# Performance work log

Measured on AMD Instinct MI355X. Metric: run time of the kernel, lower is better.

Reference implementation:

```python
import jax, jax.numpy as jnp
import numpy as np

N_NODES = 100000
N_EDGES = 250000
IN_CH = 256
OUT_CH = 256
REL_DIM = 1536
N_REL = 64
HIDDEN = IN_CH * 2  # 512
EPS = 1e-5


def setup_inputs() -> dict:
    key = jax.random.key(0)
    ks = jax.random.split(key, 12)
    s = 0.02
    return {
        "x": jax.random.normal(ks[0], (N_NODES, IN_CH), jnp.float32),
        "edge_index": jax.random.randint(ks[1], (2, N_EDGES), 0, N_NODES, jnp.int64),
        "edge_type": jax.random.randint(ks[2], (N_EDGES,), 0, N_REL, jnp.int64),
        "relation_embs": jax.random.normal(ks[3], (N_REL, REL_DIM), jnp.float32),
        "W1": jax.random.normal(ks[4], (IN_CH + REL_DIM, HIDDEN), jnp.float32) * s,
        "b1": jnp.zeros((HIDDEN,), jnp.float32),
        "W2": jax.random.normal(ks[5], (HIDDEN, OUT_CH), jnp.float32) * s,
        "b2": jnp.zeros((OUT_CH,), jnp.float32),
        "Ws": jax.random.normal(ks[6], (IN_CH, OUT_CH), jnp.float32) * s,
        "bs": jnp.zeros((OUT_CH,), jnp.float32),
        "gamma": jnp.ones((OUT_CH,), jnp.float32),
        "beta": jnp.zeros((OUT_CH,), jnp.float32),
    }


def reference(x, edge_index, edge_type, relation_embs, W1, b1, W2, b2, Ws, bs, gamma, beta):
    src, dst = edge_index[0], edge_index[1]
    # gather: per-edge inputs [E, in+rel]
    msg_in = jnp.concatenate([x[src], relation_embs[edge_type]], axis=-1)
    # message MLP: Linear -> ReLU -> Linear
    h = jax.nn.relu(msg_in @ W1 + b1)
    messages = h @ W2 + b2  # [E, out]
    # scatter_add into destination nodes
    agg = jax.ops.segment_sum(messages, dst, num_segments=x.shape[0])
    out = x @ Ws + bs + agg
    # LayerNorm (eps=1e-5) then ReLU
    mu = jnp.mean(out, axis=-1, keepdims=True)
    var = jnp.mean(jnp.square(out - mu), axis=-1, keepdims=True)
    out = (out - mu) * jax.lax.rsqrt(var + EPS) * gamma + beta
    return jax.nn.relu(out)
```

## Files before the change

### kernel.cpp

```cpp
#include <hip/hip_runtime.h>
#include <hip/hip_bf16.h>

#define IN_CHN 256
#define OUT_CHN 256
#define REL_DIM 1536
#define HIDN 512

using short8 = __attribute__((ext_vector_type(8))) short;
using f32x4  = __attribute__((ext_vector_type(4))) float;

__device__ __forceinline__ float bf2f(short s) {
    union { unsigned u; float f; } v;
    v.u = ((unsigned)(unsigned short)s) << 16;
    return v.f;
}
__device__ __forceinline__ unsigned cvt_pk_bf16(float a, float b) {
    unsigned r;
    asm("v_cvt_pk_bf16_f32 %0, %1, %2" : "=v"(r) : "v"(a), "v"(b));
    return r;
}
__device__ __forceinline__ unsigned short f2bf_s(float f) {
    union { float f; unsigned u; } v; v.f = f;
    unsigned u = v.u + 0x7FFFu + ((v.u >> 16) & 1u);
    return (unsigned short)(u >> 16);
}

__global__ void k_prep_w(const float* __restrict__ W1, const float* __restrict__ Ws,
                         const float* __restrict__ W2,
                         unsigned short* __restrict__ Bt, unsigned short* __restrict__ W2t,
                         unsigned short* __restrict__ Wst)
{
    int idx = blockIdx.x * 256 + threadIdx.x;
    const int n1 = HIDN * IN_CHN;
    const int n2 = OUT_CHN * HIDN;
    const int n3 = OUT_CHN * IN_CHN;
    if (idx < n1) {
        int j = idx >> 8, k = idx & 255;
        Bt[idx] = f2bf_s(W1[(size_t)k * HIDN + j]);
    } else if (idx < n1 + n2) {
        int t = idx - n1;
        int j = t >> 9, k = t & 511;
        W2t[t] = f2bf_s(W2[(size_t)k * OUT_CHN + j]);
    } else if (idx < n1 + n2 + n3) {
        int t = idx - n1 - n2;
        int j = t >> 8, k = t & 255;
        Wst[t] = f2bf_s(Ws[(size_t)k * OUT_CHN + j]);
    }
}

__global__ __launch_bounds__(512) void k_rel(const float* __restrict__ rel,
                                             const float* __restrict__ W1,
                                             const float* __restrict__ b1,
                                             unsigned short* __restrict__ Rb)
{
    __shared__ float s[REL_DIM];
    const int r = blockIdx.x;
    for (int i = threadIdx.x; i < REL_DIM; i += 512)
        s[i] = rel[(size_t)r * REL_DIM + i];
    __syncthreads();
    const int j = threadIdx.x;
    float acc = b1[j];
    const float* wp = W1 + (size_t)IN_CHN * HIDN + j;
#pragma unroll 8
    for (int k = 0; k < REL_DIM; ++k)
        acc = fmaf(s[k], wp[(size_t)k * HIDN], acc);
    Rb[r * HIDN + j] = f2bf_s(acc);
}

__global__ __launch_bounds__(256) void k_node(const float* __restrict__ x,
                                              const unsigned short* __restrict__ Bt,
                                              unsigned short* __restrict__ X1, int N)
{
    __shared__ unsigned short Alds[64][72];
    const int row0 = blockIdx.x * 64;
    const int colb = blockIdx.y * 256;
    const int tid = threadIdx.x;
    const int w = tid >> 6, l = tid & 63;
    const int l15 = l & 15, lg = l >> 4;
    const int colw = colb + w * 64;

    const int srow = tid >> 2;
    int srowg = row0 + srow; if (srowg >= N) srowg = N - 1;
    const int sc = (tid & 3) * 16;
    const float* xsrc = x + (size_t)srowg * IN_CHN + sc;
    unsigned short* sdst0 = &Alds[srow][sc];
    unsigned short* sdst1 = &Alds[srow][sc + 8];

    const unsigned short* bp[4];
#pragma unroll
    for (int cf = 0; cf < 4; ++cf)
        bp[cf] = Bt + (size_t)(colw + 16 * cf + l15) * IN_CHN + 8 * lg;
    const unsigned short* ard[4];
#pragma unroll
    for (int rf = 0; rf < 4; ++rf)
        ard[rf] = &Alds[16 * rf + l15][lg * 8];

    f32x4 acc[4][4] = {};

    {
        float4 f0 = *(const float4*)(xsrc + 0);
        float4 f1 = *(const float4*)(xsrc + 4);
        float4 f2 = *(const float4*)(xsrc + 8);
        float4 f3 = *(const float4*)(xsrc + 12);
        union { short8 s; unsigned u[4]; } p0, p1;
        p0.u[0] = cvt_pk_bf16(f0.x, f0.y); p0.u[1] = cvt_pk_bf16(f0.z, f0.w);
        p0.u[2] = cvt_pk_bf16(f1.x, f1.y); p0.u[3] = cvt_pk_bf16(f1.z, f1.w);
        p1.u[0] = cvt_pk_bf16(f2.x, f2.y); p1.u[1] = cvt_pk_bf16(f2.z, f2.w);
        p1.u[2] = cvt_pk_bf16(f3.x, f3.y); p1.u[3] = cvt_pk_bf16(f3.z, f3.w);
        *(short8*)sdst0 = p0.s;
        *(short8*)sdst1 = p1.s;
    }
    __syncthreads();
    for (int t = 0; t < 4; ++t) {
        float4 f0, f1, f2, f3;
        if (t + 1 < 4) {
            f0 = *(const float4*)(xsrc + (t + 1) * 64);
            f1 = *(const float4*)(xsrc + (t + 1) * 64 + 4);
            f2 = *(const float4*)(xsrc + (t + 1) * 64 + 8);
            f3 = *(const float4*)(xsrc + (t + 1) * 64 + 12);
        }
#pragma unroll
        for (int kk = 0; kk < 2; ++kk) {
            short8 a[4], b[4];
#pragma unroll
            for (int rf = 0; rf < 4; ++rf)
                a[rf] = *(const short8*)(ard[rf] + kk * 32);
#pragma unroll
            for (int cf = 0; cf < 4; ++cf)
                b[cf] = *(const short8*)(bp[cf] + t * 64 + kk * 32);
#pragma unroll
            for (int rf = 0; rf < 4; ++rf)
#pragma unroll
                for (int cf = 0; cf < 4; ++cf)
                    acc[rf][cf] = __builtin_amdgcn_mfma_f32_16x16x32_bf16(a[rf], b[cf], acc[rf][cf], 0, 0, 0);
        }
        __syncthreads();
        if (t + 1 < 4) {
            union { short8 s; unsigned u[4]; } p0, p1;
            p0.u[0] = cvt_pk_bf16(f0.x, f0.y); p0.u[1] = cvt_pk_bf16(f0.z, f0.w);
            p0.u[2] = cvt_pk_bf16(f1.x, f1.y); p0.u[3] = cvt_pk_bf16(f1.z, f1.w);
            p1.u[0] = cvt_pk_bf16(f2.x, f2.y); p1.u[1] = cvt_pk_bf16(f2.z, f2.w);
            p1.u[2] = cvt_pk_bf16(f3.x, f3.y); p1.u[3] = cvt_pk_bf16(f3.z, f3.w);
            *(short8*)sdst0 = p0.s;
            *(short8*)sdst1 = p1.s;
            __syncthreads();
        }
    }

#pragma unroll
    for (int rf = 0; rf < 4; ++rf) {
#pragma unroll
        for (int cf = 0; cf < 4; ++cf) {
            int col = colw + 16 * cf + l15;
#pragma unroll
            for (int r = 0; r < 4; ++r) {
                int row = row0 + 16 * rf + 4 * lg + r;
                if (row >= N) continue;
                X1[(size_t)row * HIDN + col] = f2bf_s(acc[rf][cf][r]);
            }
        }
    }
}

__global__ void k_hist(const int* __restrict__ ei, int* __restrict__ cnt, int E)
{
    int e = blockIdx.x * 256 + threadIdx.x;
    if (e < E) atomicAdd(&cnt[ei[E + e]], 1);
}

__global__ __launch_bounds__(512) void k_scan1(const int* __restrict__ cnt, int* __restrict__ offs,
                                               int* __restrict__ bsum, int N)
{
    __shared__ int s[512];
    int t = threadIdx.x;
    int i = blockIdx.x * 512 + t;
    int v = (i < N) ? cnt[i] : 0;
    s[t] = v;
    __syncthreads();
    for (int d = 1; d < 512; d <<= 1) {
        int a = (t >= d) ? s[t - d] : 0;
        __syncthreads();
        s[t] += a;
        __syncthreads();
    }
    if (i < N) offs[i] = s[t] - v;
    if (t == 511) bsum[blockIdx.x] = s[511];
}

__global__ __launch_bounds__(512) void k_scan2(int* __restrict__ bsum, int NB)
{
    __shared__ int s[512];
    int t = threadIdx.x;
    if (t < NB) s[t] = bsum[t];
    __syncthreads();
    if (t == 0) {
        int run = 0;
        for (int j = 0; j < NB; ++j) { int v = s[j]; s[j] = run; run += v; }
    }
    __syncthreads();
    if (t < NB) bsum[t] = s[t];
}

__global__ void k_scan3(int* __restrict__ offs, const int* __restrict__ bsum,
                        int* __restrict__ cursor, int N, int E)
{
    int i = blockIdx.x * 256 + threadIdx.x;
    if (i < N) {
        int v = offs[i] + bsum[i >> 9];
        offs[i] = v;
        cursor[i] = v;
    }
    if (i == 0) offs[N] = E;
}

__global__ void k_scatter(const int* __restrict__ ei, const int* __restrict__ et,
                          int* __restrict__ cursor, int* __restrict__ eperm, int E)
{
    int e = blockIdx.x * 256 + threadIdx.x;
    if (e < E) {
        int d = ei[E + e];
        int pos = atomicAdd(&cursor[d], 1);
        eperm[pos] = ei[e] | (et[e] << 20);
    }
}

__global__ __launch_bounds__(256, 6) void k_gather(const int* __restrict__ offs,
                                                   const int* __restrict__ eperm,
                                                   const unsigned short* __restrict__ X1,
                                                   const unsigned short* __restrict__ Rb,
                                                   unsigned short* __restrict__ Hagg, int N)
{
    const int g = (blockIdx.x * 256 + threadIdx.x) >> 6;
    const int l = threadIdx.x & 63;
    if (g >= N) return;
    const int o0 = offs[g], o1 = offs[g + 1];
    const int deg = o1 - o0;
    float a8[8] = {};
    for (int base = 0; base < deg; base += 64) {
        const int nk = min(64, deg - base);
        int pv = eperm[o0 + base + (l < nk ? l : nk - 1)];
        for (int e = 0; e < nk; e += 4) {
            int pvk[4];
#pragma unroll
            for (int k2 = 0; k2 < 4; ++k2)
                pvk[k2] = __shfl(pv, e + k2);
            short8 xa[4], ra[4];
#pragma unroll
            for (int k2 = 0; k2 < 4; ++k2) {
                if (e + k2 < nk) {
                    xa[k2] = *(const short8*)(X1 + (size_t)(pvk[k2] & 0xFFFFF) * HIDN + l * 8);
                    ra[k2] = *(const short8*)(Rb + (pvk[k2] >> 20) * HIDN + l * 8);
                }
            }
#pragma unroll
            for (int k2 = 0; k2 < 4; ++k2) {
                if (e + k2 < nk) {
#pragma unroll
                    for (int j = 0; j < 8; ++j)
                        a8[j] += fmaxf(bf2f(xa[k2][j]) + bf2f(ra[k2][j]), 0.f);
                }
            }
        }
    }
    union { short8 s; unsigned u[4]; } pk;
    pk.u[0] = cvt_pk_bf16(a8[0], a8[1]);
    pk.u[1] = cvt_pk_bf16(a8[2], a8[3]);
    pk.u[2] = cvt_pk_bf16(a8[4], a8[5]);
    pk.u[3] = cvt_pk_bf16(a8[6], a8[7]);
    *(short8*)(Hagg + (size_t)g * HIDN + l * 8) = pk.s;
}

__global__ __launch_bounds__(256) void k_out(const unsigned short* __restrict__ Hagg,
                                             const unsigned short* __restrict__ W2t,
                                             const unsigned short* __restrict__ Wst,
                                             const float* __restrict__ x,
                                             const int* __restrict__ offs,
                                             const float* __restrict__ b2,
                                             const float* __restrict__ bs,
                                             const float* __restrict__ gamma,
                                             const float* __restrict__ beta,
                                             float* __restrict__ out, int N)
{
    __shared__ unsigned short Alds[64][72];
    __shared__ float sdeg[64];
    __shared__ float sred[4][64], sqred[4][64];
    const int row0 = blockIdx.x * 64;
    const int tid = threadIdx.x;
    const int w = tid >> 6, l = tid & 63;
    const int l15 = l & 15, lg = l >> 4;
    const int colw = w * 64;

    if (tid < 64) {
        int g = row0 + tid;
        if (g >= N) g = N - 1;
        sdeg[tid] = (float)(offs[g + 1] - offs[g]);
    }

    const int srow = tid >> 2;
    int srowg = row0 + srow; if (srowg >= N) srowg = N - 1;
    const int sc = (tid & 3) * 16;
    const unsigned short* hsrc = Hagg + (size_t)srowg * HIDN + sc;
    const float* xsrc = x + (size_t)srowg * IN_CHN + sc;
    unsigned short* sdst0 = &Alds[srow][sc];
    unsigned short* sdst1 = &Alds[srow][sc + 8];

    const unsigned short* bp[4];
    const unsigned short* sp[4];
#pragma unroll
    for (int cf = 0; cf < 4; ++cf) {
        bp[cf] = W2t + (size_t)(colw + 16 * cf + l15) * HIDN + 8 * lg;
        sp[cf] = Wst + (size_t)(colw + 16 * cf + l15) * IN_CHN + 8 * lg;
    }
    const unsigned short* ard[4];
#pragma unroll
    for (int rf = 0; rf < 4; ++rf)
        ard[rf] = &Alds[16 * rf + l15][lg * 8];

    f32x4 acc[4][4] = {};
    short8 st0, st1;

    st0 = *(const short8*)(hsrc + 0);
    st1 = *(const short8*)(hsrc + 8);
    *(short8*)sdst0 = st0;
    *(short8*)sdst1 = st1;
    __syncthreads();
    for (int t = 0; t < 8; ++t) {
        if (t + 1 < 8) {
            st0 = *(const short8*)(hsrc + (t + 1) * 64);
            st1 = *(const short8*)(hsrc + (t + 1) * 64 + 8);
        }
#pragma unroll
        for (int kk = 0; kk < 2; ++kk) {
            short8 a[4], b[4];
#pragma unroll
            for (int rf = 0; rf < 4; ++rf)
                a[rf] = *(const short8*)(ard[rf] + kk * 32);
#pragma unroll
            for (int cf = 0; cf < 4; ++cf)
                b[cf] = *(const short8*)(bp[cf] + t * 64 + kk * 32);
#pragma unroll
            for (int rf = 0; rf < 4; ++rf)
#pragma unroll
                for (int cf = 0; cf < 4; ++cf)
                    acc[rf][cf] = __builtin_amdgcn_mfma_f32_16x16x32_bf16(a[rf], b[cf], acc[rf][cf], 0, 0, 0);
        }
        __syncthreads();
        if (t + 1 < 8) {
            *(short8*)sdst0 = st0;
            *(short8*)sdst1 = st1;
            __syncthreads();
        }
    }

    {
        float4 f0 = *(const float4*)(xsrc + 0);
        float4 f1 = *(const float4*)(xsrc + 4);
        float4 f2 = *(const float4*)(xsrc + 8);
        float4 f3 = *(const float4*)(xsrc + 12);
        union { short8 s; unsigned u[4]; } p0, p1;
        p0.u[0] = cvt_pk_bf16(f0.x, f0.y); p0.u[1] = cvt_pk_bf16(f0.z, f0.w);
        p0.u[2] = cvt_pk_bf16(f1.x, f1.y); p0.u[3] = cvt_pk_bf16(f1.z, f1.w);
        p1.u[0] = cvt_pk_bf16(f2.x, f2.y); p1.u[1] = cvt_pk_bf16(f2.z, f2.w);
        p1.u[2] = cvt_pk_bf16(f3.x, f3.y); p1.u[3] = cvt_pk_bf16(f3.z, f3.w);
        *(short8*)sdst0 = p0.s;
        *(short8*)sdst1 = p1.s;
    }
    __syncthreads();
    for (int t = 0; t < 4; ++t) {
        float4 f0, f1, f2, f3;
        if (t + 1 < 4) {
            f0 = *(const float4*)(xsrc + (t + 1) * 64);
            f1 = *(const float4*)(xsrc + (t + 1) * 64 + 4);
            f2 = *(const float4*)(xsrc + (t + 1) * 64 + 8);
            f3 = *(const float4*)(xsrc + (t + 1) * 64 + 12);
        }
#pragma unroll
        for (int kk = 0; kk < 2; ++kk) {
            short8 a[4], b[4];
#pragma unroll
            for (int rf = 0; rf < 4; ++rf)
                a[rf] = *(const short8*)(ard[rf] + kk * 32);
#pragma unroll
            for (int cf = 0; cf < 4; ++cf)
                b[cf] = *(const short8*)(sp[cf] + t * 64 + kk * 32);
#pragma unroll
            for (int rf = 0; rf < 4; ++rf)
#pragma unroll
                for (int cf = 0; cf < 4; ++cf)
                    acc[rf][cf] = __builtin_amdgcn_mfma_f32_16x16x32_bf16(a[rf], b[cf], acc[rf][cf], 0, 0, 0);
        }
        __syncthreads();
        if (t + 1 < 4) {
            union { short8 s; unsigned u[4]; } p0, p1;
            p0.u[0] = cvt_pk_bf16(f0.x, f0.y); p0.u[1] = cvt_pk_bf16(f0.z, f0.w);
            p0.u[2] = cvt_pk_bf16(f1.x, f1.y); p0.u[3] = cvt_pk_bf16(f1.z, f1.w);
            p1.u[0] = cvt_pk_bf16(f2.x, f2.y); p1.u[1] = cvt_pk_bf16(f2.z, f2.w);
            p1.u[2] = cvt_pk_bf16(f3.x, f3.y); p1.u[3] = cvt_pk_bf16(f3.z, f3.w);
            *(short8*)sdst0 = p0.s;
            *(short8*)sdst1 = p1.s;
            __syncthreads();
        }
    }

    float b2v[4], bsv[4], gv[4], bv[4];
#pragma unroll
    for (int cf = 0; cf < 4; ++cf) {
        int col = colw + 16 * cf + l15;
        b2v[cf] = b2[col]; bsv[cf] = bs[col]; gv[cf] = gamma[col]; bv[cf] = beta[col];
    }
#pragma unroll
    for (int rf = 0; rf < 4; ++rf) {
#pragma unroll
        for (int r = 0; r < 4; ++r) {
            int row = 16 * rf + 4 * lg + r;
            float dg = sdeg[row];
            float s = 0.f, sq = 0.f;
#pragma unroll
            for (int cf = 0; cf < 4; ++cf) {
                float v = acc[rf][cf][r] + dg * b2v[cf] + bsv[cf];
                acc[rf][cf][r] = v;
                s += v; sq += v * v;
            }
#pragma unroll
            for (int o = 8; o > 0; o >>= 1) {
                s  += __shfl_xor(s, o);
                sq += __shfl_xor(sq, o);
            }
            if (l15 == 0) { sred[w][row] = s; sqred[w][row] = sq; }
        }
    }
    __syncthreads();
#pragma unroll
    for (int rf = 0; rf < 4; ++rf) {
#pragma unroll
        for (int r = 0; r < 4; ++r) {
            int row = 16 * rf + 4 * lg + r;
            int g = row0 + row;
            if (g >= N) continue;
            float tot  = sred[0][row] + sred[1][row] + sred[2][row] + sred[3][row];
            float totq = sqred[0][row] + sqred[1][row] + sqred[2][row] + sqred[3][row];
            float mu = tot * (1.f / OUT_CHN);
            float var = totq * (1.f / OUT_CHN) - mu * mu;
            float rstd = rsqrtf(var + 1e-5f);
#pragma unroll
            for (int cf = 0; cf < 4; ++cf) {
                int col = colw + 16 * cf + l15;
                float v = (acc[rf][cf][r] - mu) * rstd * gv[cf] + bv[cf];
                out[(size_t)g * OUT_CHN + col] = fmaxf(v, 0.f);
            }
        }
    }
}

extern "C" void kernel_launch(void* const* d_in, const int* in_sizes, int n_in,
                              void* d_out, int out_size, void* d_ws, size_t ws_size,
                              hipStream_t stream)
{
    const float* x     = (const float*)d_in[0];
    const int*   ei    = (const int*)d_in[1];
    const int*   etype = (const int*)d_in[2];
    const float* rel   = (const float*)d_in[3];
    const float* W1    = (const float*)d_in[4];
    const float* b1    = (const float*)d_in[5];
    const float* W2    = (const float*)d_in[6];
    const float* b2    = (const float*)d_in[7];
    const float* Ws    = (const float*)d_in[8];
    const float* bs    = (const float*)d_in[9];
    const float* gamma = (const float*)d_in[10];
    const float* beta  = (const float*)d_in[11];

    const int N  = in_sizes[0] / IN_CHN;
    const int E  = in_sizes[2];
    const int NR = in_sizes[3] / REL_DIM;
    float* outp = (float*)d_out;

    char* wsp = (char*)d_ws;
    auto carve = [&](size_t bytes) { char* p = wsp; wsp += (bytes + 255) & ~(size_t)255; return p; };
    unsigned short* X1  = (unsigned short*)carve((size_t)N * HIDN * 2);
    unsigned short* Rb  = (unsigned short*)carve((size_t)NR * HIDN * 2);
    unsigned short* Bt  = (unsigned short*)carve((size_t)HIDN * IN_CHN * 2);
    unsigned short* W2t = (unsigned short*)carve((size_t)OUT_CHN * HIDN * 2);
    unsigned short* Wst = (unsigned short*)carve((size_t)OUT_CHN * IN_CHN * 2);
    int* offs  = (int*)carve(((size_t)N + 1) * 4);
    int* cnt   = (int*)carve((size_t)N * 4);
    int* bsum  = (int*)carve(512 * 4);
    int* eperm = (int*)carve((size_t)E * 4);

    unsigned short* Hagg = (unsigned short*)d_out;

    hipMemsetAsync(cnt, 0, (size_t)N * 4, stream);

    const int prep_total = HIDN * IN_CHN + OUT_CHN * HIDN + OUT_CHN * IN_CHN;
    k_prep_w<<<dim3((prep_total + 255) / 256), dim3(256), 0, stream>>>(W1, Ws, W2, Bt, W2t, Wst);
    k_rel<<<dim3(NR), dim3(512), 0, stream>>>(rel, W1, b1, Rb);
    k_node<<<dim3((N + 63) / 64, 2), dim3(256), 0, stream>>>(x, Bt, X1, N);
    k_hist<<<dim3((E + 255) / 256), dim3(256), 0, stream>>>(ei, cnt, E);
    int NB = (N + 511) / 512;
    k_scan1<<<dim3(NB), dim3(512), 0, stream>>>(cnt, offs, bsum, N);
    k_scan2<<<dim3(1), dim3(512), 0, stream>>>(bsum, NB);
    k_scan3<<<dim3((N + 255) / 256), dim3(256), 0, stream>>>(offs, bsum, cnt, N, E);
    k_scatter<<<dim3((E + 255) / 256), dim3(256), 0, stream>>>(ei, etype, cnt, eperm, E);
    k_gather<<<dim3((N + 3) / 4), dim3(256), 0, stream>>>(offs, eperm, X1, Rb, Hagg, N);
    k_out<<<dim3((N + 63) / 64), dim3(256), 0, stream>>>(Hagg, W2t, Wst, x, offs,
                                                         b2, bs, gamma, beta, outp, N);
}
```

Before: 431.7 us.

## Enlarge per-block tiles in node and output GEMMs to share operand staging

k_node now uses one 512-thread block per 64 rows that covers all 512 hidden columns, where before it used two 256-thread blocks. Each x row is therefore loaded and converted to bf16 only once instead of twice. k_out now processes 128 rows per 512-thread block with a 2x4 wave grid, so each W2t/Wst fragment load feeds two row groups and per-row launch overhead shrinks. The trade-off is larger blocks, fewer blocks in the grid and higher register and LDS use per block, which could lower occupancy.

After: 460.7 us. +6.7%, slower.

```diff
diff --git a/kernel.cpp b/kernel.cpp
--- a/kernel.cpp
+++ b/kernel.cpp
@@ -67,35 +67,279 @@
     Rb[r * HIDN + j] = f2bf_s(acc);
 }
 
-__global__ __launch_bounds__(256) void k_node(const float* __restrict__ x,
+__global__ __launch_bounds__(512) void k_node(const float* __restrict__ x,
                                               const unsigned short* __restrict__ Bt,
                                               unsigned short* __restrict__ X1, int N)
 {
     __shared__ unsigned short Alds[64][72];
     const int row0 = blockIdx.x * 64;
-    const int colb = blockIdx.y * 256;
     const int tid = threadIdx.x;
     const int w = tid >> 6, l = tid & 63;
     const int l15 = l & 15, lg = l >> 4;
-    const int colw = colb + w * 64;
+    const int colw = w * 64;
+
+    const int srow = tid >> 3;
+    int srowg = row0 + srow; if (srowg >= N) srowg = N - 1;
+    const int sc = (tid & 7) * 8;
+    const float* xsrc = x + (size_t)srowg * IN_CHN + sc;
+    unsigned short* sdst = &Alds[srow][sc];
+
+    const unsigned short* bp[4];
+#pragma unroll
+    for (int cf = 0; cf < 4; ++cf)
+        bp[cf] = Bt + (size_t)(colw + 16 * cf + l15) * IN_CHN + 8 * lg;
+    const unsigned short* ard[4];
+#pragma unroll
+    for (int rf = 0; rf < 4; ++rf)
+        ard[rf] = &Alds[16 * rf + l15][lg * 8];
+
+    f32x4 acc[4][4] = {};
+
+    {
+        float4 g0 = *(const float4*)(xsrc + 0);
+        float4 g1 = *(const float4*)(xsrc + 4);
+        union { short8 s; unsigned u[4]; } p;
+        p.u[0] = cvt_pk_bf16(g0.x, g0.y); p.u[1] = cvt_pk_bf16(g0.z, g0.w);
+        p.u[2] = cvt_pk_bf16(g1.x, g1.y); p.u[3] = cvt_pk_bf16(g1.z, g1.w);
+        *(short8*)sdst = p.s;
+    }
+    __syncthreads();
+    for (int t = 0; t < 4; ++t) {
+        float4 g0, g1;
+        if (t + 1 < 4) {
+            g0 = *(const float4*)(xsrc + (t + 1) * 64);
+            g1 = *(const float4*)(xsrc + (t + 1) * 64 + 4);
+        }
+#pragma unroll
+        for (int kk = 0; kk < 2; ++kk) {
+            short8 a[4], b[4];
+#pragma unroll
+            for (int rf = 0; rf < 4; ++rf)
+                a[rf] = *(const short8*)(ard[rf] + kk * 32);
+#pragma unroll
+            for (int cf = 0; cf < 4; ++cf)
+                b[cf] = *(const short8*)(bp[cf] + t * 64 + kk * 32);
+#pragma unroll
+            for (int rf = 0; rf < 4; ++rf)
+#pragma unroll
+                for (int cf = 0; cf < 4; ++cf)
+                    acc[rf][cf] = __builtin_amdgcn_mfma_f32_16x16x32_bf16(a[rf], b[cf], acc[rf][cf], 0, 0, 0);
+        }
+        __syncthreads();
+        if (t + 1 < 4) {
+            union { short8 s; unsigned u[4]; } p;
+            p.u[0] = cvt_pk_bf16(g0.x, g0.y); p.u[1] = cvt_pk_bf16(g0.z, g0.w);
+            p.u[2] = cvt_pk_bf16(g1.x, g1.y); p.u[3] = cvt_pk_bf16(g1.z, g1.w);
+            *(short8*)sdst = p.s;
+            __syncthreads();
+        }
+    }
+
+#pragma unroll
+    for (int rf = 0; rf < 4; ++rf) {
+#pragma unroll
+        for (int cf = 0; cf < 4; ++cf) {
+            int col = colw + 16 * cf + l15;
+#pragma unroll
+            for (int r = 0; r < 4; ++r) {
+                int row = row0 + 16 * rf + 4 * lg + r;
+                if (row >= N) continue;
+                X1[(size_t)row * HIDN + col] = f2bf_s(acc[rf][cf][r]);
+            }
+        }
+    }
+}
+
+__global__ void k_hist(const int* __restrict__ ei, int* __restrict__ cnt, int E)
+{
+    int e = blockIdx.x * 256 + threadIdx.x;
+    if (e < E) atomicAdd(&cnt[ei[E + e]], 1);
+}
+
+__global__ __launch_bounds__(512) void k_scan1(const int* __restrict__ cnt, int* __restrict__ offs,
+                                               int* __restrict__ bsum, int N)
+{
+    __shared__ int s[512];
+    int t = threadIdx.x;
+    int i = blockIdx.x * 512 + t;
+    int v = (i < N) ? cnt[i] : 0;
+    s[t] = v;
+    __syncthreads();
+    for (int d = 1; d < 512; d <<= 1) {
+        int a = (t >= d) ? s[t - d] : 0;
+        __syncthreads();
+        s[t] += a;
+        __syncthreads();
+    }
+    if (i < N) offs[i] = s[t] - v;
+    if (t == 511) bsum[blockIdx.x] = s[511];
+}
+
+__global__ __launch_bounds__(512) void k_scan2(int* __restrict__ bsum, int NB)
+{
+    __shared__ int s[512];
+    int t = threadIdx.x;
+    if (t < NB) s[t] = bsum[t];
+    __syncthreads();
+    if (t == 0) {
+        int run = 0;
+        for (int j = 0; j < NB; ++j) { int v = s[j]; s[j] = run; run += v; }
+    }
+    __syncthreads();
+    if (t < NB) bsum[t] = s[t];
+}
+
+__global__ void k_scan3(int* __restrict__ offs, const int* __restrict__ bsum,
+                        int* __restrict__ cursor, int N, int E)
+{
+    int i = blockIdx.x * 256 + threadIdx.x;
+    if (i < N) {
+        int v = offs[i] + bsum[i >> 9];
+        offs[i] = v;
+        cursor[i] = v;
+    }
+    if (i == 0) offs[N] = E;
+}
+
+__global__ void k_scatter(const int* __restrict__ ei, const int* __restrict__ et,
+                          int* __restrict__ cursor, int* __restrict__ eperm, int E)
+{
+    int e = blockIdx.x * 256 + threadIdx.x;
+    if (e < E) {
+        int d = ei[E + e];
+        int pos = atomicAdd(&cursor[d], 1);
+        eperm[pos] = ei[e] | (et[e] << 20);
+    }
+}
+
+__global__ __launch_bounds__(256, 6) void k_gather(const int* __restrict__ offs,
+                                                   const int* __restrict__ eperm,
+                                                   const unsigned short* __restrict__ X1,
+                                                   const unsigned short* __restrict__ Rb,
+                                                   unsigned short* __restrict__ Hagg, int N)
+{
+    const int g = (blockIdx.x * 256 + threadIdx.x) >> 6;
+    const int l = threadIdx.x & 63;
+    if (g >= N) return;
+    const int o0 = offs[g], o1 = offs[g + 1];
+    const int deg = o1 - o0;
+    float a8[8] = {};
+    for (int base = 0; base < deg; base += 64) {
+        const int nk = min(64, deg - base);
+        int pv = eperm[o0 + base + (l < nk ? l : nk - 1)];
+        for (int e = 0; e < nk; e += 4) {
+            int pvk[4];
+#pragma unroll
+            for (int k2 = 0; k2 < 4; ++k2)
+                pvk[k2] = __shfl(pv, e + k2);
+            short8 xa[4], ra[4];
+#pragma unroll
+            for (int k2 = 0; k2 < 4; ++k2) {
+                if (e + k2 < nk) {
+                    xa[k2] = *(const short8*)(X1 + (size_t)(pvk[k2] & 0xFFFFF) * HIDN + l * 8);
+                    ra[k2] = *(const short8*)(Rb + (pvk[k2] >> 20) * HIDN + l * 8);
+                }
+            }
+#pragma unroll
+            for (int k2 = 0; k2 < 4; ++k2) {
+                if (e + k2 < nk) {
+#pragma unroll
+                    for (int j = 0; j < 8; ++j)
+                        a8[j] += fmaxf(bf2f(xa[k2][j]) + bf2f(ra[k2][j]), 0.f);
+                }
+            }
+        }
+    }
+    union { short8 s; unsigned u[4]; } pk;
+    pk.u[0] = cvt_pk_bf16(a8[0], a8[1]);
+    pk.u[1] = cvt_pk_bf16(a8[2], a8[3]);
+    pk.u[2] = cvt_pk_bf16(a8[4], a8[5]);
+    pk.u[3] = cvt_pk_bf16(a8[6], a8[7]);
+    *(short8*)(Hagg + (size_t)g * HIDN + l * 8) = pk.s;
+}
+
+__global__ __launch_bounds__(512) void k_out(const unsigned short* __restrict__ Hagg,
+                                             const unsigned short* __restrict__ W2t,
+                                             const unsigned short* __restrict__ Wst,
+                                             const float* __restrict__ x,
+                                             const int* __restrict__ offs,
+                                             const float* __restrict__ b2,
+                                             const float* __restrict__ bs,
+                                             const float* __restrict__ gamma,
+                                             const float* __restrict__ beta,
+                                             float* __restrict__ out, int N)
+{
+    __shared__ unsigned short Alds[128][72];
+    __shared__ float sdeg[128];
+    __shared__ float sred[4][128], sqred[4][128];
+    const int row0 = blockIdx.x * 128;
+    const int tid = threadIdx.x;
+    const int w = tid >> 6, l = tid & 63;
+    const int wr = w >> 2, wc = w & 3;
+    const int l15 = l & 15, lg = l >> 4;
+    const int colw = wc * 64;
+
+    if (tid < 128) {
+        int g = row0 + tid;
+        if (g >= N) g = N - 1;
+        sdeg[tid] = (float)(offs[g + 1] - offs[g]);
+    }
 
     const int srow = tid >> 2;
     int srowg = row0 + srow; if (srowg >= N) srowg = N - 1;
     const int sc = (tid & 3) * 16;
+    const unsigned short* hsrc = Hagg + (size_t)srowg * HIDN + sc;
     const float* xsrc = x + (size_t)srowg * IN_CHN + sc;
     unsigned short* sdst0 = &Alds[srow][sc];
     unsigned short* sdst1 = &Alds[srow][sc + 8];
 
     const unsigned short* bp[4];
-#pragma unroll
-    for (int cf = 0; cf < 4; ++cf)
-        bp[cf] = Bt + (size_t)(colw + 16 * cf + l15) * IN_CHN + 8 * lg;
+    const unsigned short* sp[4];
+#pragma unroll
+    for (int cf = 0; cf < 4; ++cf) {
+        bp[cf] = W2t + (size_t)(colw + 16 * cf + l15) * HIDN + 8 * lg;
+        sp[cf] = Wst + (size_t)(colw + 16 * cf + l15) * IN_CHN + 8 * lg;
+    }
     const unsigned short* ard[4];
 #pragma unroll
     for (int rf = 0; rf < 4; ++rf)
-        ard[rf] = &Alds[16 * rf + l15][lg * 8];
+        ard[rf] = &Alds[wr * 64 + 16 * rf + l15][lg * 8];
 
     f32x4 acc[4][4] = {};
+    short8 st0, st1;
+
+    st0 = *(const short8*)(hsrc + 0);
+    st1 = *(const short8*)(hsrc + 8);
+    *(short8*)sdst0 = st0;
+    *(short8*)sdst1 = st1;
+    __syncthreads();
+    for (int t = 0; t < 8; ++t) {
+        if (t + 1 < 8) {
+            st0 = *(const short8*)(hsrc + (t + 1) * 64);
+            st1 = *(const short8*)(hsrc + (t + 1) * 64 + 8);
+        }
+#pragma unroll
+        for (int kk = 0; kk < 2; ++kk) {
+            short8 a[4], b[4];
+#pragma unroll
+            for (int rf = 0; rf < 4; ++rf)
+                a[rf] = *(const short8*)(ard[rf] + kk * 32);
+#pragma unroll
+            for (int cf = 0; cf < 4; ++cf)
+                b[cf] = *(const short8*)(bp[cf] + t * 64 + kk * 32);
+#pragma unroll
+            for (int rf = 0; rf < 4; ++rf)
+#pragma unroll
+                for (int cf = 0; cf < 4; ++cf)
+                    acc[rf][cf] = __builtin_amdgcn_mfma_f32_16x16x32_bf16(a[rf], b[cf], acc[rf][cf], 0, 0, 0);
+        }
+        __syncthreads();
+        if (t + 1 < 8) {
+            *(short8*)sdst0 = st0;
+            *(short8*)sdst1 = st1;
+            __syncthreads();
+        }
+    }
 
     {
         float4 f0 = *(const float4*)(xsrc + 0);
@@ -127,7 +371,7 @@
                 a[rf] = *(const short8*)(ard[rf] + kk * 32);
 #pragma unroll
             for (int cf = 0; cf < 4; ++cf)
-                b[cf] = *(const short8*)(bp[cf] + t * 64 + kk * 32);
+                b[cf] = *(const short8*)(sp[cf] + t * 64 + kk * 32);
 #pragma unroll
             for (int rf = 0; rf < 4; ++rf)
 #pragma unroll
@@ -147,261 +391,6 @@
         }
     }
 
-#pragma unroll
-    for (int rf = 0; rf < 4; ++rf) {
-#pragma unroll
-        for (int cf = 0; cf < 4; ++cf) {
-            int col = colw + 16 * cf + l15;
-#pragma unroll
-            for (int r = 0; r < 4; ++r) {
-                int row = row0 + 16 * rf + 4 * lg + r;
-                if (row >= N) continue;
-                X1[(size_t)row * HIDN + col] = f2bf_s(acc[rf][cf][r]);
-            }
-        }
-    }
-}
-
-__global__ void k_hist(const int* __restrict__ ei, int* __restrict__ cnt, int E)
-{
-    int e = blockIdx.x * 256 + threadIdx.x;
-    if (e < E) atomicAdd(&cnt[ei[E + e]], 1);
-}
-
-__global__ __launch_bounds__(512) void k_scan1(const int* __restrict__ cnt, int* __restrict__ offs,
-                                               int* __restrict__ bsum, int N)
-{
-    __shared__ int s[512];
-    int t = threadIdx.x;
-    int i = blockIdx.x * 512 + t;
-    int v = (i < N) ? cnt[i] : 0;
-    s[t] = v;
-    __syncthreads();
-    for (int d = 1; d < 512; d <<= 1) {
-        int a = (t >= d) ? s[t - d] : 0;
-        __syncthreads();
-        s[t] += a;
-        __syncthreads();
-    }
-    if (i < N) offs[i] = s[t] - v;
-    if (t == 511) bsum[blockIdx.x] = s[511];
-}
-
-__global__ __launch_bounds__(512) void k_scan2(int* __restrict__ bsum, int NB)
-{
-    __shared__ int s[512];
-    int t = threadIdx.x;
-    if (t < NB) s[t] = bsum[t];
-    __syncthreads();
-    if (t == 0) {
-        int run = 0;
-        for (int j = 0; j < NB; ++j) { int v = s[j]; s[j] = run; run += v; }
-    }
-    __syncthreads();
-    if (t < NB) bsum[t] = s[t];
-}
-
-__global__ void k_scan3(int* __restrict__ offs, const int* __restrict__ bsum,
-                        int* __restrict__ cursor, int N, int E)
-{
-    int i = blockIdx.x * 256 + threadIdx.x;
-    if (i < N) {
-        int v = offs[i] + bsum[i >> 9];
-        offs[i] = v;
-        cursor[i] = v;
-    }
-    if (i == 0) offs[N] = E;
-}
-
-__global__ void k_scatter(const int* __restrict__ ei, const int* __restrict__ et,
-                          int* __restrict__ cursor, int* __restrict__ eperm, int E)
-{
-    int e = blockIdx.x * 256 + threadIdx.x;
-    if (e < E) {
-        int d = ei[E + e];
-        int pos = atomicAdd(&cursor[d], 1);
-        eperm[pos] = ei[e] | (et[e] << 20);
-    }
-}
-
-__global__ __launch_bounds__(256, 6) void k_gather(const int* __restrict__ offs,
-                                                   const int* __restrict__ eperm,
-                                                   const unsigned short* __restrict__ X1,
-                                                   const unsigned short* __restrict__ Rb,
-                                                   unsigned short* __restrict__ Hagg, int N)
-{
-    const int g = (blockIdx.x * 256 + threadIdx.x) >> 6;
-    const int l = threadIdx.x & 63;
-    if (g >= N) return;
-    const int o0 = offs[g], o1 = offs[g + 1];
-    const int deg = o1 - o0;
-    float a8[8] = {};
-    for (int base = 0; base < deg; base += 64) {
-        const int nk = min(64, deg - base);
-        int pv = eperm[o0 + base + (l < nk ? l : nk - 1)];
-        for (int e = 0; e < nk; e += 4) {
-            int pvk[4];
-#pragma unroll
-            for (int k2 = 0; k2 < 4; ++k2)
-                pvk[k2] = __shfl(pv, e + k2);
-            short8 xa[4], ra[4];
-#pragma unroll
-            for (int k2 = 0; k2 < 4; ++k2) {
-                if (e + k2 < nk) {
-                    xa[k2] = *(const short8*)(X1 + (size_t)(pvk[k2] & 0xFFFFF) * HIDN + l * 8);
-                    ra[k2] = *(const short8*)(Rb + (pvk[k2] >> 20) * HIDN + l * 8);
-                }
-            }
-#pragma unroll
-            for (int k2 = 0; k2 < 4; ++k2) {
-                if (e + k2 < nk) {
-#pragma unroll
-                    for (int j = 0; j < 8; ++j)
-                        a8[j] += fmaxf(bf2f(xa[k2][j]) + bf2f(ra[k2][j]), 0.f);
-                }
-            }
-        }
-    }
-    union { short8 s; unsigned u[4]; } pk;
-    pk.u[0] = cvt_pk_bf16(a8[0], a8[1]);
-    pk.u[1] = cvt_pk_bf16(a8[2], a8[3]);
-    pk.u[2] = cvt_pk_bf16(a8[4], a8[5]);
-    pk.u[3] = cvt_pk_bf16(a8[6], a8[7]);
-    *(short8*)(Hagg + (size_t)g * HIDN + l * 8) = pk.s;
-}
-
-__global__ __launch_bounds__(256) void k_out(const unsigned short* __restrict__ Hagg,
-                                             const unsigned short* __restrict__ W2t,
-                                             const unsigned short* __restrict__ Wst,
-                                             const float* __restrict__ x,
-                                             const int* __restrict__ offs,
-                                             const float* __restrict__ b2,
-                                             const float* __restrict__ bs,
-                                             const float* __restrict__ gamma,
-                                             const float* __restrict__ beta,
-                                             float* __restrict__ out, int N)
-{
-    __shared__ unsigned short Alds[64][72];
-    __shared__ float sdeg[64];
-    __shared__ float sred[4][64], sqred[4][64];
-    const int row0 = blockIdx.x * 64;
-    const int tid = threadIdx.x;
-    const int w = tid >> 6, l = tid & 63;
-    const int l15 = l & 15, lg = l >> 4;
-    const int colw = w * 64;
-
-    if (tid < 64) {
-        int g = row0 + tid;
-        if (g >= N) g = N - 1;
-        sdeg[tid] = (float)(offs[g + 1] - offs[g]);
-    }
-
-    const int srow = tid >> 2;
-    int srowg = row0 + srow; if (srowg >= N) srowg = N - 1;
-    const int sc = (tid & 3) * 16;
-    const unsigned short* hsrc = Hagg + (size_t)srowg * HIDN + sc;
-    const float* xsrc = x + (size_t)srowg * IN_CHN + sc;
-    unsigned short* sdst0 = &Alds[srow][sc];
-    unsigned short* sdst1 = &Alds[srow][sc + 8];
-
-    const unsigned short* bp[4];
-    const unsigned short* sp[4];
-#pragma unroll
-    for (int cf = 0; cf < 4; ++cf) {
-        bp[cf] = W2t + (size_t)(colw + 16 * cf + l15) * HIDN + 8 * lg;
-        sp[cf] = Wst + (size_t)(colw + 16 * cf + l15) * IN_CHN + 8 * lg;
-    }
-    const unsigned short* ard[4];
-#pragma unroll
-    for (int rf = 0; rf < 4; ++rf)
-        ard[rf] = &Alds[16 * rf + l15][lg * 8];
-
-    f32x4 acc[4][4] = {};
-    short8 st0, st1;
-
-    st0 = *(const short8*)(hsrc + 0);
-    st1 = *(const short8*)(hsrc + 8);
-    *(short8*)sdst0 = st0;
-    *(short8*)sdst1 = st1;
-    __syncthreads();
-    for (int t = 0; t < 8; ++t) {
-        if (t + 1 < 8) {
-            st0 = *(const short8*)(hsrc + (t + 1) * 64);
-            st1 = *(const short8*)(hsrc + (t + 1) * 64 + 8);
-        }
-#pragma unroll
-        for (int kk = 0; kk < 2; ++kk) {
-            short8 a[4], b[4];
-#pragma unroll
-            for (int rf = 0; rf < 4; ++rf)
-                a[rf] = *(const short8*)(ard[rf] + kk * 32);
-#pragma unroll
-            for (int cf = 0; cf < 4; ++cf)
-                b[cf] = *(const short8*)(bp[cf] + t * 64 + kk * 32);
-#pragma unroll
-            for (int rf = 0; rf < 4; ++rf)
-#pragma unroll
-                for (int cf = 0; cf < 4; ++cf)
-                    acc[rf][cf] = __builtin_amdgcn_mfma_f32_16x16x32_bf16(a[rf], b[cf], acc[rf][cf], 0, 0, 0);
-        }
-        __syncthreads();
-        if (t + 1 < 8) {
-            *(short8*)sdst0 = st0;
-            *(short8*)sdst1 = st1;
-            __syncthreads();
-        }
-    }
-
-    {
-        float4 f0 = *(const float4*)(xsrc + 0);
-        float4 f1 = *(const float4*)(xsrc + 4);
-        float4 f2 = *(const float4*)(xsrc + 8);
-        float4 f3 = *(const float4*)(xsrc + 12);
-        union { short8 s; unsigned u[4]; } p0, p1;
-        p0.u[0] = cvt_pk_bf16(f0.x, f0.y); p0.u[1] = cvt_pk_bf16(f0.z, f0.w);
-        p0.u[2] = cvt_pk_bf16(f1.x, f1.y); p0.u[3] = cvt_pk_bf16(f1.z, f1.w);
-        p1.u[0] = cvt_pk_bf16(f2.x, f2.y); p1.u[1] = cvt_pk_bf16(f2.z, f2.w);
-        p1.u[2] = cvt_pk_bf16(f3.x, f3.y); p1.u[3] = cvt_pk_bf16(f3.z, f3.w);
-        *(short8*)sdst0 = p0.s;
-        *(short8*)sdst1 = p1.s;
-    }
-    __syncthreads();
-    for (int t = 0; t < 4; ++t) {
-        float4 f0, f1, f2, f3;
-        if (t + 1 < 4) {
-            f0 = *(const float4*)(xsrc + (t + 1) * 64);
-            f1 = *(const float4*)(xsrc + (t + 1) * 64 + 4);
-            f2 = *(const float4*)(xsrc + (t + 1) * 64 + 8);
-            f3 = *(const float4*)(xsrc + (t + 1) * 64 + 12);
-        }
-#pragma unroll
-        for (int kk = 0; kk < 2; ++kk) {
-            short8 a[4], b[4];
-#pragma unroll
-            for (int rf = 0; rf < 4; ++rf)
-                a[rf] = *(const short8*)(ard[rf] + kk * 32);
-#pragma unroll
-            for (int cf = 0; cf < 4; ++cf)
-                b[cf] = *(const short8*)(sp[cf] + t * 64 + kk * 32);
-#pragma unroll
-            for (int rf = 0; rf < 4; ++rf)
-#pragma unroll
-                for (int cf = 0; cf < 4; ++cf)
-                    acc[rf][cf] = __builtin_amdgcn_mfma_f32_16x16x32_bf16(a[rf], b[cf], acc[rf][cf], 0, 0, 0);
-        }
-        __syncthreads();
-        if (t + 1 < 4) {
-            union { short8 s; unsigned u[4]; } p0, p1;
-            p0.u[0] = cvt_pk_bf16(f0.x, f0.y); p0.u[1] = cvt_pk_bf16(f0.z, f0.w);
-            p0.u[2] = cvt_pk_bf16(f1.x, f1.y); p0.u[3] = cvt_pk_bf16(f1.z, f1.w);
-            p1.u[0] = cvt_pk_bf16(f2.x, f2.y); p1.u[1] = cvt_pk_bf16(f2.z, f2.w);
-            p1.u[2] = cvt_pk_bf16(f3.x, f3.y); p1.u[3] = cvt_pk_bf16(f3.z, f3.w);
-            *(short8*)sdst0 = p0.s;
-            *(short8*)sdst1 = p1.s;
-            __syncthreads();
-        }
-    }
-
     float b2v[4], bsv[4], gv[4], bv[4];
 #pragma unroll
     for (int cf = 0; cf < 4; ++cf) {
@@ -412,7 +401,7 @@
     for (int rf = 0; rf < 4; ++rf) {
 #pragma unroll
         for (int r = 0; r < 4; ++r) {
-            int row = 16 * rf + 4 * lg + r;
+            int row = wr * 64 + 16 * rf + 4 * lg + r;
             float dg = sdeg[row];
             float s = 0.f, sq = 0.f;
 #pragma unroll
@@ -426,7 +415,7 @@
                 s  += __shfl_xor(s, o);
                 sq += __shfl_xor(sq, o);
             }
-            if (l15 == 0) { sred[w][row] = s; sqred[w][row] = sq; }
+            if (l15 == 0) { sred[wc][row] = s; sqred[wc][row] = sq; }
         }
     }
     __syncthreads();
@@ -434,7 +423,7 @@
     for (int rf = 0; rf < 4; ++rf) {
 #pragma unroll
         for (int r = 0; r < 4; ++r) {
-            int row = 16 * rf + 4 * lg + r;
+            int row = wr * 64 + 16 * rf + 4 * lg + r;
             int g = row0 + row;
             if (g >= N) continue;
             float tot  = sred[0][row] + sred[1][row] + sred[2][row] + sred[3][row];
@@ -493,7 +482,7 @@
     const int prep_total = HIDN * IN_CHN + OUT_CHN * HIDN + OUT_CHN * IN_CHN;
     k_prep_w<<<dim3((prep_total + 255) / 256), dim3(256), 0, stream>>>(W1, Ws, W2, Bt, W2t, Wst);
     k_rel<<<dim3(NR), dim3(512), 0, stream>>>(rel, W1, b1, Rb);
-    k_node<<<dim3((N + 63) / 64, 2), dim3(256), 0, stream>>>(x, Bt, X1, N);
+    k_node<<<dim3((N + 63) / 64), dim3(512), 0, stream>>>(x, Bt, X1, N);
     k_hist<<<dim3((E + 255) / 256), dim3(256), 0, stream>>>(ei, cnt, E);
     int NB = (N + 511) / 512;
     k_scan1<<<dim3(NB), dim3(512), 0, stream>>>(cnt, offs, bsum, N);
@@ -501,6 +490,6 @@
     k_scan3<<<dim3((N + 255) / 256), dim3(256), 0, stream>>>(offs, bsum, cnt, N, E);
     k_scatter<<<dim3((E + 255) / 256), dim3(256), 0, stream>>>(ei, etype, cnt, eperm, E);
     k_gather<<<dim3((N + 3) / 4), dim3(256), 0, stream>>>(offs, eperm, X1, Rb, Hagg, N);
-    k_out<<<dim3((N + 63) / 64), dim3(256), 0, stream>>>(Hagg, W2t, Wst, x, offs,
-                                                         b2, bs, gamma, beta, outp, N);
-}
+    k_out<<<dim3((N + 127) / 128), dim3(512), 0, stream>>>(Hagg, W2t, Wst, x, offs,
+                                                           b2, bs, gamma, beta, outp, N);
+}
```
